# Performance work log

Hardware: AMD Instinct MI355X
Metric: run time of the kernel (lower is better)

The kernel has to match this reference:

```python
import jax, jax.numpy as jnp
import numpy as np

DIM, HEADS, K_MAX, K_MIN = 512, 8, 32, 4
DH = DIM // HEADS


def _conv1x1(x, w, b=None):
    # 1x1 Conv2d == pointwise linear over channels: [B,C,H,W] x [O,C] -> [B,O,H,W]
    y = jnp.einsum('bchw,oc->bohw', x, w)
    if b is not None:
        y = y + b[None, :, None, None]
    return y


def setup_inputs() -> dict:
    key = jax.random.key(0)
    ks = jax.random.split(key, 8)
    B, C, H, W = 2, DIM, 64, 64
    s = lambda fan: 1.0 / np.sqrt(fan)
    x = jax.random.normal(ks[0], (B, C, H, W), jnp.float32)
    w_qkv = jax.random.normal(ks[1], (3 * C, C), jnp.float32) * s(C)   # qkv conv, bias=False
    w_proj = jax.random.normal(ks[2], (C, C), jnp.float32) * s(C)      # proj conv
    b_proj = jax.random.normal(ks[3], (C,), jnp.float32) * s(C)
    w_g1 = jax.random.normal(ks[4], (C // 4, C), jnp.float32) * s(C)   # gate conv 1
    b_g1 = jax.random.normal(ks[5], (C // 4,), jnp.float32) * s(C)
    w_g2 = jax.random.normal(ks[6], (1, C // 4), jnp.float32) * s(C // 4)  # gate conv 2
    b_g2 = jnp.full((1,), -1.0, jnp.float32)  # nn.init.constant_(gate[-2].bias, -1.0)
    return {"x": x, "w_qkv": w_qkv, "w_proj": w_proj, "b_proj": b_proj,
            "w_g1": w_g1, "b_g1": b_g1, "w_g2": w_g2, "b_g2": b_g2}


def reference(x, w_qkv, w_proj, b_proj, w_g1, b_g1, w_g2, b_g2):
    B, C, H, W = x.shape
    N = H * W
    qkv = _conv1x1(x, w_qkv)                              # [B,3C,H,W]
    q, k, v = jnp.split(qkv, 3, axis=1)

    def rs(t):  # [B,C,H,W] -> [B,heads,N,dh]
        return t.reshape(B, HEADS, DH, N).transpose(0, 1, 3, 2)

    q, k, v = rs(q), rs(k), rs(v)
    sim = jnp.einsum('bhid,bhjd->bhij', q, k) / np.sqrt(DH)  # [B,h,N,N]

    # adaptive tau gate -> per-query dynamic k
    tau = jax.nn.sigmoid(_conv1x1(jax.nn.relu(_conv1x1(x, w_g1, b_g1)), w_g2, b_g2))
    tau = tau.reshape(B, 1, N)
    k_dyn = jnp.clip((tau * K_MAX).astype(jnp.int32), K_MIN, K_MAX)  # [B,1,N]

    topk_val, topk_idx = jax.lax.top_k(sim, K_MAX)         # [B,h,N,K], sorted descending
    mask = jnp.arange(K_MAX)[None, None, None, :] < k_dyn[..., None]  # [B,1,N,K] (bcast over h)
    topk_val = jnp.where(mask, topk_val, -jnp.inf)
    attn = jax.nn.softmax(topk_val, axis=-1)               # [B,h,N,K]

    # gather values: gathered[b,h,i,kk,:] = v[b,h,topk_idx[b,h,i,kk],:]
    bi = jnp.arange(B)[:, None, None, None]
    hi = jnp.arange(HEADS)[None, :, None, None]
    gathered = v[bi, hi, topk_idx]                         # [B,h,N,K,dh]
    out = jnp.einsum('bhnk,bhnkd->bhnd', attn, gathered)   # [B,h,N,dh]

    out = out.transpose(0, 1, 3, 2).reshape(B, C, H, W)
    out = _conv1x1(out, w_proj, b_proj)                    # proj (proj_drop=0)
    return x + out
```

## Files before the change

### kernel.cpp

```cpp
#include <hip/hip_runtime.h>
#include <math.h>

#define XSTRIDE  2097152u
#define G1STRIDE 524288u

typedef _Float16 f16;
typedef f16   f16x8  __attribute__((ext_vector_type(8)));
typedef float f32x16 __attribute__((ext_vector_type(16)));
typedef unsigned int u32;
typedef unsigned short u16;

#define WS_QH 0u
#define WS_QL 2097152u
#define WS_KH 4194304u
#define WS_KL 6291456u
#define WS_VB 8388608u
#define WS_G1 10485760u
#define WS_KD 11534336u
#define WS_CI 11542528u

template<int EPI>
__global__ __launch_bounds__(256)
void gemm_kernel(const float* __restrict__ A, const float* __restrict__ B,
                 const float* __restrict__ bias, const float* __restrict__ resid,
                 void* P0, void* P1, void* P2, void* P3, void* P4)
{
    const int tid = threadIdx.x;
    const int tm = tid & 15;
    const int tn = tid >> 4;
    const int m0 = blockIdx.y * 128;
    const int n0 = blockIdx.x * 128;
    const int b  = blockIdx.z;

    const float* Bb = B + (size_t)b * XSTRIDE;

    __shared__ float As[16][132];
    __shared__ float Bs[16][132];

    float acc[8][8];
    #pragma unroll
    for (int i = 0; i < 8; ++i)
        #pragma unroll
        for (int j = 0; j < 8; ++j) acc[i][j] = 0.0f;

    for (int k0 = 0; k0 < 512; k0 += 16) {
        {
            int id = tid * 2;
            #pragma unroll
            for (int r = 0; r < 2; ++r, ++id) {
                int m = id >> 2, kq = (id & 3) * 4;
                float4 v = *(const float4*)(A + (size_t)(m0 + m) * 512 + k0 + kq);
                As[kq + 0][m] = v.x; As[kq + 1][m] = v.y;
                As[kq + 2][m] = v.z; As[kq + 3][m] = v.w;
            }
        }
        if (EPI != 2) {
            int id = tid * 2;
            #pragma unroll
            for (int r = 0; r < 2; ++r, ++id) {
                int kk = id >> 5, nq = (id & 31) * 4;
                *(float4*)(&Bs[kk][nq]) =
                    *(const float4*)(Bb + (size_t)(k0 + kk) * 4096 + n0 + nq);
            }
        } else {
            const float* O0p = (const float*)P1;
            const float* O1p = (const float*)P2;
            const int hh = k0 >> 6, d0 = k0 & 63;
            int id = tid * 2;
            #pragma unroll
            for (int r = 0; r < 2; ++r, ++id) {
                int n = id >> 2, kq = (id & 3) * 4;
                int dd = d0 + kq;
                size_t rowp = ((size_t)((b * 8 + hh) * 4096) + n0 + n) * 32;
                const float* src = (dd < 32) ? (O0p + rowp + dd) : (O1p + rowp + dd - 32);
                float4 v = *(const float4*)src;
                Bs[kq + 0][n] = v.x; Bs[kq + 1][n] = v.y;
                Bs[kq + 2][n] = v.z; Bs[kq + 3][n] = v.w;
            }
        }
        __syncthreads();
        #pragma unroll
        for (int k = 0; k < 16; ++k) {
            float4 a0 = *(const float4*)(&As[k][tm * 8]);
            float4 a1 = *(const float4*)(&As[k][tm * 8 + 4]);
            float4 b0 = *(const float4*)(&Bs[k][tn * 8]);
            float4 b1 = *(const float4*)(&Bs[k][tn * 8 + 4]);
            float a[8] = {a0.x, a0.y, a0.z, a0.w, a1.x, a1.y, a1.z, a1.w};
            float bb[8] = {b0.x, b0.y, b0.z, b0.w, b1.x, b1.y, b1.z, b1.w};
            #pragma unroll
            for (int i = 0; i < 8; ++i)
                #pragma unroll
                for (int j = 0; j < 8; ++j)
                    acc[i][j] += a[i] * bb[j];
        }
        __syncthreads();
    }

    if (EPI == 2) {
        float* out = (float*)P0;
        #pragma unroll
        for (int i = 0; i < 8; ++i) {
            int o = m0 + tm * 8 + i;
            float bi = bias[o];
            size_t off = (size_t)b * XSTRIDE + (size_t)o * 4096 + n0 + tn * 8;
            float4 r0 = *(const float4*)(resid + off);
            float4 r1 = *(const float4*)(resid + off + 4);
            *(float4*)(out + off) = make_float4(acc[i][0] + bi + r0.x, acc[i][1] + bi + r0.y,
                                                acc[i][2] + bi + r0.z, acc[i][3] + bi + r0.w);
            *(float4*)(out + off + 4) = make_float4(acc[i][4] + bi + r1.x, acc[i][5] + bi + r1.y,
                                                    acc[i][6] + bi + r1.z, acc[i][7] + bi + r1.w);
        }
    }
}

__global__ __launch_bounds__(256)
void gate1_kernel(const float* __restrict__ A,
                  const float* __restrict__ B,
                  const float* __restrict__ bias,
                  float* __restrict__ G1)
{
    const int tid = threadIdx.x;
    const int tm = tid & 15;
    const int tn = tid >> 4;
    const int n0 = blockIdx.x * 32;
    const int b  = blockIdx.z;
    const float* Bb = B + (size_t)b * XSTRIDE;

    __shared__ float As[16][132];
    __shared__ float Bs[16][34];

    float acc[8][2];
    #pragma unroll
    for (int i = 0; i < 8; ++i) { acc[i][0] = 0.0f; acc[i][1] = 0.0f; }

    for (int k0 = 0; k0 < 512; k0 += 16) {
        {
            int id = tid * 2;
            #pragma unroll
            for (int r = 0; r < 2; ++r, ++id) {
                int m = id >> 2, kq = (id & 3) * 4;
                float4 v = *(const float4*)(A + (size_t)m * 512 + k0 + kq);
                As[kq + 0][m] = v.x; As[kq + 1][m] = v.y;
                As[kq + 2][m] = v.z; As[kq + 3][m] = v.w;
            }
        }
        {
            int kk = tid >> 4;
            int nn = (tid & 15) * 2;
            float2 v = *(const float2*)(Bb + (size_t)(k0 + kk) * 4096 + n0 + nn);
            Bs[kk][nn] = v.x; Bs[kk][nn + 1] = v.y;
        }
        __syncthreads();
        #pragma unroll
        for (int k = 0; k < 16; ++k) {
            float4 a0 = *(const float4*)(&As[k][tm * 8]);
            float4 a1 = *(const float4*)(&As[k][tm * 8 + 4]);
            float a[8] = {a0.x, a0.y, a0.z, a0.w, a1.x, a1.y, a1.z, a1.w};
            float b0 = Bs[k][tn * 2], b1 = Bs[k][tn * 2 + 1];
            #pragma unroll
            for (int i = 0; i < 8; ++i) {
                acc[i][0] += a[i] * b0;
                acc[i][1] += a[i] * b1;
            }
        }
        __syncthreads();
    }

    #pragma unroll
    for (int i = 0; i < 8; ++i) {
        int o = tm * 8 + i;
        float bi = bias[o];
        float* dst = G1 + (size_t)b * G1STRIDE + (size_t)o * 4096 + n0 + tn * 2;
        dst[0] = fmaxf(acc[i][0] + bi, 0.0f);
        dst[1] = fmaxf(acc[i][1] + bi, 0.0f);
    }
}

__global__ __launch_bounds__(256)
void convert_kernel(const float* __restrict__ x,
                    f16* __restrict__ XTH, f16* __restrict__ XTL)
{
    __shared__ float T[64][65];
    const int b = blockIdx.z;
    const int n0 = blockIdx.x * 64, k0 = blockIdx.y * 64;
    const int tid = threadIdx.x;
    const float* xb = x + (size_t)b * XSTRIDE;

    {
        const int c = tid & 63, r = tid >> 6;
        #pragma unroll
        for (int i = 0; i < 16; ++i)
            T[r + i * 4][c] = xb[(size_t)(k0 + r + i * 4) * 4096 + n0 + c];
    }
    __syncthreads();
    const int n = tid >> 2, a = tid & 3;
    f16x8 vh[2], vl[2];
    #pragma unroll
    for (int p = 0; p < 2; ++p)
        #pragma unroll
        for (int j = 0; j < 8; ++j) {
            float v = T[a * 16 + p * 8 + j][n];
            f16 h = (f16)v;
            vh[p][j] = h;
            vl[p][j] = (f16)((v - (float)h) * 4096.0f);
        }
    size_t dst = ((size_t)(b * 4096) + n0 + n) * 512 + k0 + a * 16;
    *(f16x8*)(XTH + dst)     = vh[0];
    *(f16x8*)(XTH + dst + 8) = vh[1];
    *(f16x8*)(XTL + dst)     = vl[0];
    *(f16x8*)(XTL + dst + 8) = vl[1];
}

__global__ __launch_bounds__(256, 2)
void qkv_gemm(const float* __restrict__ W, const f16* __restrict__ XTH,
              const f16* __restrict__ XTL,
              f16* __restrict__ QH, f16* __restrict__ QL,
              f16* __restrict__ KH, f16* __restrict__ KL,
              f16* __restrict__ VB)
{
    __shared__ __align__(16) char smem[33792];
    f16* Ah = (f16*)smem;
    f16* Al = (f16*)(smem + 6144);
    f16* Bh = (f16*)(smem + 12288);
    f16* Bl = (f16*)(smem + 18432);

    const int tid  = threadIdx.x;
    const int wid  = tid >> 6, lane = tid & 63;
    const int ln   = lane & 31, g = lane >> 5;
    const int wm   = wid >> 1, wn = wid & 1;
    const int m0   = blockIdx.y * 128;
    const int n0   = blockIdx.x * 128;
    const int b    = blockIdx.z;

    const int sm = tid >> 1, sko = (tid & 1) * 8;
    const float* wsrc  = W + (size_t)(m0 + sm) * 512 + sko;
    const f16*  bsrcH = XTH + ((size_t)(b * 4096) + n0 + sm) * 512 + sko;
    const f16*  bsrcL = XTL + ((size_t)(b * 4096) + n0 + sm) * 512 + sko;

    f32x16 accH[2][2], accL[2][2];
    #pragma unroll
    for (int rb = 0; rb < 2; ++rb)
        #pragma unroll
        for (int cb = 0; cb < 2; ++cb)
            #pragma unroll
            for (int r = 0; r < 16; ++r) { accH[rb][cb][r] = 0.0f; accL[rb][cb][r] = 0.0f; }

    for (int k0 = 0; k0 < 512; k0 += 16) {
        {
            float4 v0 = *(const float4*)(wsrc + k0);
            float4 v1 = *(const float4*)(wsrc + k0 + 4);
            float vv[8] = {v0.x, v0.y, v0.z, v0.w, v1.x, v1.y, v1.z, v1.w};
            f16x8 hh, ll;
            #pragma unroll
            for (int j = 0; j < 8; ++j) {
                f16 h = (f16)vv[j];
                hh[j] = h;
                ll[j] = (f16)((vv[j] - (float)h) * 4096.0f);
            }
            *(f16x8*)(Ah + sm * 24 + sko) = hh;
            *(f16x8*)(Al + sm * 24 + sko) = ll;
            *(f16x8*)(Bh + sm * 24 + sko) = *(const f16x8*)(bsrcH + k0);
            *(f16x8*)(Bl + sm * 24 + sko) = *(const f16x8*)(bsrcL + k0);
        }
        __syncthreads();
        f16x8 a_h[2], a_l[2], b_h[2], b_l[2];
        #pragma unroll
        for (int rb = 0; rb < 2; ++rb) {
            int row = wm * 64 + rb * 32 + ln;
            a_h[rb] = *(const f16x8*)(Ah + row * 24 + g * 8);
            a_l[rb] = *(const f16x8*)(Al + row * 24 + g * 8);
        }
        #pragma unroll
        for (int cb = 0; cb < 2; ++cb) {
            int col = wn * 64 + cb * 32 + ln;
            b_h[cb] = *(const f16x8*)(Bh + col * 24 + g * 8);
            b_l[cb] = *(const f16x8*)(Bl + col * 24 + g * 8);
        }
        #pragma unroll
        for (int rb = 0; rb < 2; ++rb)
            #pragma unroll
            for (int cb = 0; cb < 2; ++cb) {
                accH[rb][cb] = __builtin_amdgcn_mfma_f32_32x32x16_f16(a_h[rb], b_h[cb], accH[rb][cb], 0, 0, 0);
                accL[rb][cb] = __builtin_amdgcn_mfma_f32_32x32x16_f16(a_h[rb], b_l[cb], accL[rb][cb], 0, 0, 0);
                accL[rb][cb] = __builtin_amdgcn_mfma_f32_32x32x16_f16(a_l[rb], b_h[cb], accL[rb][cb], 0, 0, 0);
            }
        __syncthreads();
    }

    const int which = m0 >> 9;
    const float scale = (which == 0) ? 0.125f : 1.0f;
    const int hh_ = ((m0 & 511) >> 6) + wm;
    const size_t rowb0 = (size_t)(b * 8 + hh_) * 4096 + n0 + wn * 64 + lane;
    float* E = (float*)smem + wid * 2112;

    #pragma unroll
    for (int rb = 0; rb < 2; ++rb) {
        #pragma unroll
        for (int cb = 0; cb < 2; ++cb)
            #pragma unroll
            for (int r = 0; r < 16; ++r) {
                int row = (r & 3) + 8 * (r >> 2) + 4 * g;
                E[row * 66 + cb * 32 + ln] =
                    accH[rb][cb][r] + accL[rb][cb][r] * (1.0f / 4096.0f);
            }
        __syncthreads();
        const int dbase = rb * 32;
        if (which == 2) {
            #pragma unroll
            for (int oct = 0; oct < 4; ++oct) {
                f16x8 vv;
                #pragma unroll
                for (int j = 0; j < 8; ++j) vv[j] = (f16)E[(oct * 8 + j) * 66 + lane];
                *(f16x8*)(VB + rowb0 * 64 + dbase + oct * 8) = vv;
            }
        } else {
            f16* DH = which ? KH : QH;
            f16* DL = which ? KL : QL;
            #pragma unroll
            for (int oct = 0; oct < 4; ++oct) {
                f16x8 vh, vl;
                #pragma unroll
                for (int j = 0; j < 8; ++j) {
                    float xx = E[(oct * 8 + j) * 66 + lane] * scale;
                    f16 h = (f16)xx;
                    vh[j] = h;
                    vl[j] = (f16)((xx - (float)h) * 4096.0f);
                }
                *(f16x8*)(DH + rowb0 * 64 + dbase + oct * 8) = vh;
                *(f16x8*)(DL + rowb0 * 64 + dbase + oct * 8) = vl;
            }
        }
        __syncthreads();
    }
}

__global__ __launch_bounds__(64)
void gate2_kernel(const float* __restrict__ G1, const float* __restrict__ w2,
                  const float* __restrict__ b2, int* __restrict__ KD)
{
    const int b = blockIdx.y;
    const int n = blockIdx.x * 64 + threadIdx.x;
    const float* g = G1 + (size_t)b * G1STRIDE + n;
    float z = b2[0];
    #pragma unroll 8
    for (int c = 0; c < 128; ++c) z += w2[c] * g[(size_t)c * 4096];
    float tau = 1.0f / (1.0f + expf(-z));
    int kd = (int)(tau * 32.0f);
    kd = min(32, max(4, kd));
    KD[b * 4096 + n] = kd;
}

#define LOAD_BF(B0,B1,B2,B3,B4,B5,B6,B7, KHP, KLP, CB) do {                   \
    const f16* _ph = (KHP) + (size_t)((CB) * 32 + ln) * 64 + g * 8;           \
    const f16* _pl = (KLP) + (size_t)((CB) * 32 + ln) * 64 + g * 8;           \
    B0 = *(const f16x8*)(_ph);      B1 = *(const f16x8*)(_ph + 16);           \
    B2 = *(const f16x8*)(_ph + 32); B3 = *(const f16x8*)(_ph + 48);           \
    B4 = *(const f16x8*)(_pl);      B5 = *(const f16x8*)(_pl + 16);           \
    B6 = *(const f16x8*)(_pl + 32); B7 = *(const f16x8*)(_pl + 48);           \
} while (0)

#define P1_SCAN() do {                                                        \
    u32 _m = 0;                                                               \
    _Pragma("unroll")                                                         \
    for (int _q = 0; _q < 16; ++_q) {                                         \
        float2 _v = *(const float2*)(srow + 2 * _q);                          \
        _m |= (_v.x > thr) ? (1u << (2 * _q)) : 0u;                           \
        _m |= (_v.y > thr) ? (1u << (2 * _q + 1)) : 0u;                       \
    }                                                                         \
    while (__ballot(_m != 0u)) {                                              \
        bool _act = (_m != 0u);                                               \
        int _j = __builtin_ctz(_m ? _m : 1u);                                 \
        float _c = _act ? srow[_j] : 0.0f;                                    \
        _m &= (_m - 1u);                                                      \
        if (_act && _c > thr) {                                               \
            _Pragma("unroll")                                                 \
            for (int _r = 31; _r >= 1; --_r)                                  \
                L[_r] = __builtin_amdgcn_fmed3f(_c, L[_r - 1], L[_r]);        \
            L[0] = fmaxf(L[0], _c);                                           \
        }                                                                     \
    }                                                                         \
    {                                                                         \
        float _th = L[31];                                                    \
        _Pragma("unroll")                                                     \
        for (int _r = 30; _r >= 0; --_r) _th = (kdm1 == _r) ? L[_r] : _th;    \
        thr = _th;                                                            \
    }                                                                         \
} while (0)

#define P2_SCAN(JBASE) do {                                                   \
    u32 _m = 0;                                                               \
    _Pragma("unroll")                                                         \
    for (int _q = 0; _q < 16; ++_q) {                                         \
        float2 _v = *(const float2*)(srow + 2 * _q);                          \
        _m |= (_v.x >= theta) ? (1u << (2 * _q)) : 0u;                        \
        _m |= (_v.y >= theta) ? (1u << (2 * _q + 1)) : 0u;                    \
    }                                                                         \
    while (__ballot(_m != 0u)) {                                              \
        bool _act = (_m != 0u);                                               \
        int _j = __builtin_ctz(_m ? _m : 1u);                                 \
        float _c = _act ? srow[_j] : 0.0f;                                    \
        _m &= (_m - 1u);                                                      \
        if (_act) {                                                           \
            bool _isGT = _c > theta;                                          \
            bool _doA = (_isGT || eqc < eqNeed) && cnt < 32;                  \
            if (_doA) {                                                       \
                cvp[cnt] = _c;                                                \
                cip[cnt] = (u16)((JBASE) + _j);                               \
                cnt++;                                                        \
                if (!_isGT) eqc++;                                            \
            }                                                                 \
        }                                                                     \
    }                                                                         \
} while (0)

__device__ __forceinline__ void score_from(
    f16x8 bh0, f16x8 bh1, f16x8 bh2, f16x8 bh3,
    f16x8 bl0, f16x8 bl1, f16x8 bl2, f16x8 bl3,
    const f16x8 ah[2][4], const f16x8 al[2][4],
    float* __restrict__ Ss, int ln, int g)
{
    __builtin_amdgcn_s_setprio(1);
    #pragma unroll
    for (int rb = 0; rb < 2; ++rb) {
        f32x16 acc, accL;
        #pragma unroll
        for (int r = 0; r < 16; ++r) { acc[r] = 0.0f; accL[r] = 0.0f; }
        acc  = __builtin_amdgcn_mfma_f32_32x32x16_f16(ah[rb][0], bh0, acc,  0, 0, 0);
        accL = __builtin_amdgcn_mfma_f32_32x32x16_f16(al[rb][0], bh0, accL, 0, 0, 0);
        accL = __builtin_amdgcn_mfma_f32_32x32x16_f16(ah[rb][0], bl0, accL, 0, 0, 0);
        acc  = __builtin_amdgcn_mfma_f32_32x32x16_f16(ah[rb][1], bh1, acc,  0, 0, 0);
        accL = __builtin_amdgcn_mfma_f32_32x32x16_f16(al[rb][1], bh1, accL, 0, 0, 0);
        accL = __builtin_amdgcn_mfma_f32_32x32x16_f16(ah[rb][1], bl1, accL, 0, 0, 0);
        acc  = __builtin_amdgcn_mfma_f32_32x32x16_f16(ah[rb][2], bh2, acc,  0, 0, 0);
        accL = __builtin_amdgcn_mfma_f32_32x32x16_f16(al[rb][2], bh2, accL, 0, 0, 0);
        accL = __builtin_amdgcn_mfma_f32_32x32x16_f16(ah[rb][2], bl2, accL, 0, 0, 0);
        acc  = __builtin_amdgcn_mfma_f32_32x32x16_f16(ah[rb][3], bh3, acc,  0, 0, 0);
        accL = __builtin_amdgcn_mfma_f32_32x32x16_f16(al[rb][3], bh3, accL, 0, 0, 0);
        accL = __builtin_amdgcn_mfma_f32_32x32x16_f16(ah[rb][3], bl3, accL, 0, 0, 0);
        #pragma unroll
        for (int r = 0; r < 16; ++r) {
            int riw = rb * 32 + (r & 3) + 8 * (r >> 2) + 4 * g;
            Ss[riw * 34 + ln] = acc[r] + accL[r] * (1.0f / 4096.0f);
        }
    }
    __builtin_amdgcn_s_setprio(0);
}

__global__ __launch_bounds__(64)
__attribute__((amdgpu_waves_per_eu(2, 2)))
void select_kernel(const f16* __restrict__ QH, const f16* __restrict__ QL,
                   const f16* __restrict__ KH, const f16* __restrict__ KL,
                   const int* __restrict__ KD,
                   float* __restrict__ CV, u16* __restrict__ CI)
{
    const int qt = blockIdx.x >> 1;
    const int hf = blockIdx.x & 1;
    const int h = blockIdx.y, b = blockIdx.z;
    const size_t base = (size_t)((b * 8 + h) * 4096) * 64;
    const int lane = threadIdx.x;
    const int ln = lane & 31, g = lane >> 5;
    const int nw = qt * 64;
    const int k0base = hf * 2048;

    const int kd = KD[b * 4096 + nw + lane];
    const int kdm1 = kd - 1;

    __shared__ float Ss[64 * 34];

    f16x8 ah[2][4], al[2][4];
    #pragma unroll
    for (int rb = 0; rb < 2; ++rb) {
        const f16* ph = QH + base + (size_t)(nw + rb * 32 + ln) * 64 + g * 8;
        const f16* pl = QL + base + (size_t)(nw + rb * 32 + ln) * 64 + g * 8;
        #pragma unroll
        for (int s = 0; s < 4; ++s) {
            ah[rb][s] = *(const f16x8*)(ph + s * 16);
            al[rb][s] = *(const f16x8*)(pl + s * 16);
        }
    }

    const float INF = __builtin_inff();
    const float* srow = &Ss[lane * 34];

    f16x8 c0, c1, c2, c3, c4, c5, c6, c7;
    f16x8 n0, n1, n2, n3, n4, n5, n6, n7;

    float L[32];
    #pragma unroll
    for (int r = 0; r < 32; ++r) L[r] = -INF;
    float thr = -INF;

    {
        const f16* kh0 = KH + base + (size_t)k0base * 64;
        const f16* kl0 = KL + base + (size_t)k0base * 64;
        LOAD_BF(c0, c1, c2, c3, c4, c5, c6, c7, kh0, kl0, 0);
        for (int t = 0; t < 32; ++t) {
            const f16* kh_t = KH + base + (size_t)(k0base + t * 64) * 64;
            const f16* kl_t = KL + base + (size_t)(k0base + t * 64) * 64;
            const int t1 = (t < 31) ? t + 1 : 31;
            const f16* kh_n = KH + base + (size_t)(k0base + t1 * 64) * 64;
            const f16* kl_n = KL + base + (size_t)(k0base + t1 * 64) * 64;
            LOAD_BF(n0, n1, n2, n3, n4, n5, n6, n7, kh_t, kl_t, 1);
            score_from(c0, c1, c2, c3, c4, c5, c6, c7, ah, al, Ss, ln, g);
            P1_SCAN();
            LOAD_BF(c0, c1, c2, c3, c4, c5, c6, c7, kh_n, kl_n, 0);
            score_from(n0, n1, n2, n3, n4, n5, n6, n7, ah, al, Ss, ln, g);
            P1_SCAN();
        }
    }
    const float theta = thr;
    int cntGT = 0;
    #pragma unroll
    for (int r = 0; r < 32; ++r) cntGT += ((r < kd) && (L[r] > theta)) ? 1 : 0;
    const int eqNeed = kd - cntGT;

    const size_t crow = (size_t)((b * 8 + h) * 4096 + nw + lane);
    float* cvp = CV + crow * 64 + hf * 32;
    u16*   cip = CI + crow * 64 + hf * 32;
    int cnt = 0, eqc = 0;

    {
        const f16* kh0 = KH + base + (size_t)k0base * 64;
        const f16* kl0 = KL + base + (size_t)k0base * 64;
        LOAD_BF(c0, c1, c2, c3, c4, c5, c6, c7, kh0, kl0, 0);
        for (int t = 0; t < 32; ++t) {
            const f16* kh_t = KH + base + (size_t)(k0base + t * 64) * 64;
            const f16* kl_t = KL + base + (size_t)(k0base + t * 64) * 64;
            const int t1 = (t < 31) ? t + 1 : 31;
            const f16* kh_n = KH + base + (size_t)(k0base + t1 * 64) * 64;
            const f16* kl_n = KL + base + (size_t)(k0base + t1 * 64) * 64;
            LOAD_BF(n0, n1, n2, n3, n4, n5, n6, n7, kh_t, kl_t, 1);
            score_from(c0, c1, c2, c3, c4, c5, c6, c7, ah, al, Ss, ln, g);
            P2_SCAN(k0base + t * 64);
            LOAD_BF(c0, c1, c2, c3, c4, c5, c6, c7, kh_n, kl_n, 0);
            score_from(n0, n1, n2, n3, n4, n5, n6, n7, ah, al, Ss, ln, g);
            P2_SCAN(k0base + t * 64 + 32);
        }
    }
}

__global__ __launch_bounds__(64)
void merge_kernel(const float* __restrict__ CV, const u16* __restrict__ CI,
                  const int* __restrict__ KD, const f16* __restrict__ VB,
                  float* __restrict__ O0, float* __restrict__ O1)
{
    const int tid = threadIdx.x;
    const size_t R0 = (size_t)blockIdx.x * 64;

    __shared__ float Lv[64][66];
    __shared__ u16   Li[64][66];
    __shared__ float Mv[64][34];
    __shared__ u16   Mi[64][34];

    for (int i = 0; i < 64; ++i) {
        Lv[i][tid] = CV[(R0 + i) * 64 + tid];
        Li[i][tid] = CI[(R0 + i) * 64 + tid];
    }
    __syncthreads();

    const int myR = (int)R0 + tid;
    const int b = myR >> 15, n = myR & 4095, h = (myR >> 12) & 7;
    const int kd = KD[b * 4096 + n];

    const float INF = __builtin_inff();
    float L[32]; int I[32];
    #pragma unroll
    for (int r = 0; r < 32; ++r) { L[r] = -INF; I[r] = 0; }

    for (int i = 0; i < 64; ++i) {
        float c = Lv[tid][i];
        int  ix = Li[tid][i];
        if (c > L[31]) {
            #pragma unroll
            for (int r = 31; r >= 1; --r) {
                bool gp = c > L[r - 1];
                bool gc = c > L[r];
                L[r] = gp ? L[r - 1] : (gc ? c : L[r]);
                I[r] = gp ? I[r - 1] : (gc ? ix : I[r]);
            }
            if (c > L[0]) { I[0] = ix; L[0] = c; }
        }
    }

    #pragma unroll
    for (int r = 0; r < 32; ++r) { Mv[tid][r] = L[r]; Mi[tid][r] = (u16)I[r]; }

    const float mx = Mv[tid][0];
    float sum = 0.0f;
    for (int k = 0; k < kd; ++k) {
        float e = expf(Mv[tid][k] - mx);
        Mv[tid][k] = e;
        sum += e;
    }
    const float inv = 1.0f / sum;

    float o[64];
    #pragma unroll
    for (int d = 0; d < 64; ++d) o[d] = 0.0f;
    const size_t vbase = (size_t)((b * 8 + h)) * 4096 * 64;
    for (int k = 0; k < kd; ++k) {
        float wgt = Mv[tid][k] * inv;
        const f16* vp = VB + vbase + (size_t)Mi[tid][k] * 64;
        #pragma unroll
        for (int part = 0; part < 8; ++part) {
            f16x8 vv = *(const f16x8*)(vp + part * 8);
            #pragma unroll
            for (int e2 = 0; e2 < 8; ++e2) o[part * 8 + e2] += wgt * (float)vv[e2];
        }
    }

    __syncthreads();
    #pragma unroll
    for (int q = 0; q < 32; ++q)
        *(float2*)(&Lv[tid][2 * q]) = make_float2(o[2 * q], o[2 * q + 1]);
    __syncthreads();
    for (int i = 0; i < 64; ++i) {
        float val = Lv[i][tid];
        size_t R = R0 + i;
        if (tid < 32) O0[R * 32 + tid] = val;
        else          O1[R * 32 + (tid - 32)] = val;
    }
}

extern "C" void kernel_launch(void* const* d_in, const int* in_sizes, int n_in,
                              void* d_out, int out_size, void* d_ws, size_t ws_size,
                              hipStream_t stream)
{
    const float* x      = (const float*)d_in[0];
    const float* w_qkv  = (const float*)d_in[1];
    const float* w_proj = (const float*)d_in[2];
    const float* b_proj = (const float*)d_in[3];
    const float* w_g1   = (const float*)d_in[4];
    const float* b_g1   = (const float*)d_in[5];
    const float* w_g2   = (const float*)d_in[6];
    const float* b_g2   = (const float*)d_in[7];
    float* out = (float*)d_out;
    float* ws  = (float*)d_ws;

    f16* QH = (f16*)(ws + WS_QH);
    f16* QL = (f16*)(ws + WS_QL);
    f16* KH = (f16*)(ws + WS_KH);
    f16* KL = (f16*)(ws + WS_KL);
    f16* VB = (f16*)(ws + WS_VB);
    float* G1 = ws + WS_G1;
    int*   KD = (int*)(ws + WS_KD);
    u16*   CI = (u16*)(ws + WS_CI);
    float* CV = out;
    float* O0 = (float*)QH;
    float* O1 = (float*)QL;

    f16* XTH = (f16*)out;
    f16* XTL = (f16*)out + 4194304;

    convert_kernel<<<dim3(64, 8, 2), 256, 0, stream>>>(x, XTH, XTL);
    qkv_gemm<<<dim3(32, 12, 2), 256, 0, stream>>>(
        w_qkv, XTH, XTL, QH, QL, KH, KL, VB);
    gate1_kernel<<<dim3(128, 1, 2), 256, 0, stream>>>(w_g1, x, b_g1, G1);

    hipMemsetAsync(CV, 0xFF, (size_t)out_size * sizeof(float), stream);

    gate2_kernel<<<dim3(64, 2), 64, 0, stream>>>(G1, w_g2, b_g2, KD);
    select_kernel<<<dim3(128, 8, 2), 64, 0, stream>>>(QH, QL, KH, KL, KD, CV, CI);
    merge_kernel<<<dim3(1024), 64, 0, stream>>>(CV, CI, KD, VB, O0, O1);
    gemm_kernel<2><<<dim3(32, 4, 2), 256, 0, stream>>>(
        w_proj, nullptr, b_proj, x, out, O0, O1, nullptr, nullptr);
}
```

Before: 637.3 us.

## Move projection GEMM to split-fp16 MFMA and emit fp16 hi/lo from merge

Replaces the scalar fp32 projection GEMM with an MFMA 32x32x16 fp16 kernel that uses a hi/lo split (three MFMAs per tile) to keep near-fp32 accuracy. The merge kernel now writes its per-query outputs directly as token-major fp16 hi/lo pairs instead of staging through shared memory into two fp32 half-buffers. This is meant to cut the FMA-bound cost of the projection and simplify the merge store path. In exchange it adds an on-the-fly weight split per tile and a small precision change from the split representation.

```diff
diff --git a/kernel.cpp b/kernel.cpp
--- a/kernel.cpp
+++ b/kernel.cpp
@@ -18,100 +18,6 @@
 #define WS_G1 10485760u
 #define WS_KD 11534336u
 #define WS_CI 11542528u
-
-template<int EPI>
-__global__ __launch_bounds__(256)
-void gemm_kernel(const float* __restrict__ A, const float* __restrict__ B,
-                 const float* __restrict__ bias, const float* __restrict__ resid,
-                 void* P0, void* P1, void* P2, void* P3, void* P4)
-{
-    const int tid = threadIdx.x;
-    const int tm = tid & 15;
-    const int tn = tid >> 4;
-    const int m0 = blockIdx.y * 128;
-    const int n0 = blockIdx.x * 128;
-    const int b  = blockIdx.z;
-
-    const float* Bb = B + (size_t)b * XSTRIDE;
-
-    __shared__ float As[16][132];
-    __shared__ float Bs[16][132];
-
-    float acc[8][8];
-    #pragma unroll
-    for (int i = 0; i < 8; ++i)
-        #pragma unroll
-        for (int j = 0; j < 8; ++j) acc[i][j] = 0.0f;
-
-    for (int k0 = 0; k0 < 512; k0 += 16) {
-        {
-            int id = tid * 2;
-            #pragma unroll
-            for (int r = 0; r < 2; ++r, ++id) {
-                int m = id >> 2, kq = (id & 3) * 4;
-                float4 v = *(const float4*)(A + (size_t)(m0 + m) * 512 + k0 + kq);
-                As[kq + 0][m] = v.x; As[kq + 1][m] = v.y;
-                As[kq + 2][m] = v.z; As[kq + 3][m] = v.w;
-            }
-        }
-        if (EPI != 2) {
-            int id = tid * 2;
-            #pragma unroll
-            for (int r = 0; r < 2; ++r, ++id) {
-                int kk = id >> 5, nq = (id & 31) * 4;
-                *(float4*)(&Bs[kk][nq]) =
-                    *(const float4*)(Bb + (size_t)(k0 + kk) * 4096 + n0 + nq);
-            }
-        } else {
-            const float* O0p = (const float*)P1;
-            const float* O1p = (const float*)P2;
-            const int hh = k0 >> 6, d0 = k0 & 63;
-            int id = tid * 2;
-            #pragma unroll
-            for (int r = 0; r < 2; ++r, ++id) {
-                int n = id >> 2, kq = (id & 3) * 4;
-                int dd = d0 + kq;
-                size_t rowp = ((size_t)((b * 8 + hh) * 4096) + n0 + n) * 32;
-                const float* src = (dd < 32) ? (O0p + rowp + dd) : (O1p + rowp + dd - 32);
-                float4 v = *(const float4*)src;
-                Bs[kq + 0][n] = v.x; Bs[kq + 1][n] = v.y;
-                Bs[kq + 2][n] = v.z; Bs[kq + 3][n] = v.w;
-            }
-        }
-        __syncthreads();
-        #pragma unroll
-        for (int k = 0; k < 16; ++k) {
-            float4 a0 = *(const float4*)(&As[k][tm * 8]);
-            float4 a1 = *(const float4*)(&As[k][tm * 8 + 4]);
-            float4 b0 = *(const float4*)(&Bs[k][tn * 8]);
-            float4 b1 = *(const float4*)(&Bs[k][tn * 8 + 4]);
-            float a[8] = {a0.x, a0.y, a0.z, a0.w, a1.x, a1.y, a1.z, a1.w};
-            float bb[8] = {b0.x, b0.y, b0.z, b0.w, b1.x, b1.y, b1.z, b1.w};
-            #pragma unroll
-            for (int i = 0; i < 8; ++i)
-                #pragma unroll
-                for (int j = 0; j < 8; ++j)
-                    acc[i][j] += a[i] * bb[j];
-        }
-        __syncthreads();
-    }
-
-    if (EPI == 2) {
-        float* out = (float*)P0;
-        #pragma unroll
-        for (int i = 0; i < 8; ++i) {
-            int o = m0 + tm * 8 + i;
-            float bi = bias[o];
-            size_t off = (size_t)b * XSTRIDE + (size_t)o * 4096 + n0 + tn * 8;
-            float4 r0 = *(const float4*)(resid + off);
-            float4 r1 = *(const float4*)(resid + off + 4);
-            *(float4*)(out + off) = make_float4(acc[i][0] + bi + r0.x, acc[i][1] + bi + r0.y,
-                                                acc[i][2] + bi + r0.z, acc[i][3] + bi + r0.w);
-            *(float4*)(out + off + 4) = make_float4(acc[i][4] + bi + r1.x, acc[i][5] + bi + r1.y,
-                                                    acc[i][6] + bi + r1.z, acc[i][7] + bi + r1.w);
-        }
-    }
-}
 
 __global__ __launch_bounds__(256)
 void gate1_kernel(const float* __restrict__ A,
@@ -329,6 +235,103 @@
                 *(f16x8*)(DH + rowb0 * 64 + dbase + oct * 8) = vh;
                 *(f16x8*)(DL + rowb0 * 64 + dbase + oct * 8) = vl;
             }
+        }
+        __syncthreads();
+    }
+}
+
+__global__ __launch_bounds__(256, 2)
+void proj_gemm(const float* __restrict__ W, const f16* __restrict__ OH,
+               const f16* __restrict__ OL, const float* __restrict__ bias,
+               const float* __restrict__ resid, float* __restrict__ out)
+{
+    __shared__ __align__(16) char smem[33792];
+    f16* Ah = (f16*)smem;
+    f16* Al = (f16*)(smem + 6144);
+    f16* Bh = (f16*)(smem + 12288);
+    f16* Bl = (f16*)(smem + 18432);
+
+    const int tid  = threadIdx.x;
+    const int wid  = tid >> 6, lane = tid & 63;
+    const int ln   = lane & 31, g = lane >> 5;
+    const int wm   = wid >> 1, wn = wid & 1;
+    const int m0   = blockIdx.y * 128;
+    const int n0   = blockIdx.x * 128;
+    const int b    = blockIdx.z;
+
+    const int sm = tid >> 1, sko = (tid & 1) * 8;
+    const float* wsrc  = W + (size_t)(m0 + sm) * 512 + sko;
+    const f16*  bsrcH = OH + ((size_t)(b * 4096) + n0 + sm) * 512 + sko;
+    const f16*  bsrcL = OL + ((size_t)(b * 4096) + n0 + sm) * 512 + sko;
+
+    f32x16 accH[2][2], accL[2][2];
+    #pragma unroll
+    for (int rb = 0; rb < 2; ++rb)
+        #pragma unroll
+        for (int cb = 0; cb < 2; ++cb)
+            #pragma unroll
+            for (int r = 0; r < 16; ++r) { accH[rb][cb][r] = 0.0f; accL[rb][cb][r] = 0.0f; }
+
+    for (int k0 = 0; k0 < 512; k0 += 16) {
+        {
+            float4 v0 = *(const float4*)(wsrc + k0);
+            float4 v1 = *(const float4*)(wsrc + k0 + 4);
+            float vv[8] = {v0.x, v0.y, v0.z, v0.w, v1.x, v1.y, v1.z, v1.w};
+            f16x8 hh, ll;
+            #pragma unroll
+            for (int j = 0; j < 8; ++j) {
+                f16 h = (f16)vv[j];
+                hh[j] = h;
+                ll[j] = (f16)((vv[j] - (float)h) * 4096.0f);
+            }
+            *(f16x8*)(Ah + sm * 24 + sko) = hh;
+            *(f16x8*)(Al + sm * 24 + sko) = ll;
+            *(f16x8*)(Bh + sm * 24 + sko) = *(const f16x8*)(bsrcH + k0);
+            *(f16x8*)(Bl + sm * 24 + sko) = *(const f16x8*)(bsrcL + k0);
+        }
+        __syncthreads();
+        f16x8 a_h[2], a_l[2], b_h[2], b_l[2];
+        #pragma unroll
+        for (int rb = 0; rb < 2; ++rb) {
+            int row = wm * 64 + rb * 32 + ln;
+            a_h[rb] = *(const f16x8*)(Ah + row * 24 + g * 8);
+            a_l[rb] = *(const f16x8*)(Al + row * 24 + g * 8);
+        }
+        #pragma unroll
+        for (int cb = 0; cb < 2; ++cb) {
+            int col = wn * 64 + cb * 32 + ln;
+            b_h[cb] = *(const f16x8*)(Bh + col * 24 + g * 8);
+            b_l[cb] = *(const f16x8*)(Bl + col * 24 + g * 8);
+        }
+        #pragma unroll
+        for (int rb = 0; rb < 2; ++rb)
+            #pragma unroll
+            for (int cb = 0; cb < 2; ++cb) {
+                accH[rb][cb] = __builtin_amdgcn_mfma_f32_32x32x16_f16(a_h[rb], b_h[cb], accH[rb][cb], 0, 0, 0);
+                accL[rb][cb] = __builtin_amdgcn_mfma_f32_32x32x16_f16(a_h[rb], b_l[cb], accL[rb][cb], 0, 0, 0);
+                accL[rb][cb] = __builtin_amdgcn_mfma_f32_32x32x16_f16(a_l[rb], b_h[cb], accL[rb][cb], 0, 0, 0);
+            }
+        __syncthreads();
+    }
+
+    float* E = (float*)smem + wid * 2112;
+    #pragma unroll
+    for (int rb = 0; rb < 2; ++rb) {
+        #pragma unroll
+        for (int cb = 0; cb < 2; ++cb)
+            #pragma unroll
+            for (int r = 0; r < 16; ++r) {
+                int row = (r & 3) + 8 * (r >> 2) + 4 * g;
+                E[row * 66 + cb * 32 + ln] =
+                    accH[rb][cb][r] + accL[rb][cb][r] * (1.0f / 4096.0f);
+            }
+        __syncthreads();
+        #pragma unroll 4
+        for (int r = 0; r < 32; ++r) {
+            int o = m0 + wm * 64 + rb * 32 + r;
+            size_t off = (size_t)b * XSTRIDE + (size_t)o * 4096
+                       + n0 + wn * 64 + lane;
+            out[off] = E[r * 66 + lane] + bias[o] + resid[off];
         }
         __syncthreads();
     }
@@ -542,7 +545,7 @@
 __global__ __launch_bounds__(64)
 void merge_kernel(const float* __restrict__ CV, const u16* __restrict__ CI,
                   const int* __restrict__ KD, const f16* __restrict__ VB,
-                  float* __restrict__ O0, float* __restrict__ O1)
+                  f16* __restrict__ OH, f16* __restrict__ OL)
 {
     const int tid = threadIdx.x;
     const size_t R0 = (size_t)blockIdx.x * 64;
@@ -609,16 +612,19 @@
         }
     }
 
-    __syncthreads();
-    #pragma unroll
-    for (int q = 0; q < 32; ++q)
-        *(float2*)(&Lv[tid][2 * q]) = make_float2(o[2 * q], o[2 * q + 1]);
-    __syncthreads();
-    for (int i = 0; i < 64; ++i) {
-        float val = Lv[i][tid];
-        size_t R = R0 + i;
-        if (tid < 32) O0[R * 32 + tid] = val;
-        else          O1[R * 32 + (tid - 32)] = val;
+    const size_t obase = ((size_t)(b * 4096) + n) * 512 + h * 64;
+    #pragma unroll
+    for (int part = 0; part < 8; ++part) {
+        f16x8 vh, vl;
+        #pragma unroll
+        for (int e2 = 0; e2 < 8; ++e2) {
+            float v = o[part * 8 + e2];
+            f16 hh = (f16)v;
+            vh[e2] = hh;
+            vl[e2] = (f16)((v - (float)hh) * 4096.0f);
+        }
+        *(f16x8*)(OH + obase + part * 8) = vh;
+        *(f16x8*)(OL + obase + part * 8) = vl;
     }
 }
 
@@ -646,8 +652,8 @@
     int*   KD = (int*)(ws + WS_KD);
     u16*   CI = (u16*)(ws + WS_CI);
     float* CV = out;
-    float* O0 = (float*)QH;
-    float* O1 = (float*)QL;
+    f16* OH = (f16*)QH;
+    f16* OL = (f16*)QL;
 
     f16* XTH = (f16*)out;
     f16* XTL = (f16*)out + 4194304;
@@ -661,7 +667,7 @@
 
     gate2_kernel<<<dim3(64, 2), 64, 0, stream>>>(G1, w_g2, b_g2, KD);
     select_kernel<<<dim3(128, 8, 2), 64, 0, stream>>>(QH, QL, KH, KL, KD, CV, CI);
-    merge_kernel<<<dim3(1024), 64, 0, stream>>>(CV, CI, KD, VB, O0, O1);
-    gemm_kernel<2><<<dim3(32, 4, 2), 256, 0, stream>>>(
-        w_proj, nullptr, b_proj, x, out, O0, O1, nullptr, nullptr);
-}
+    merge_kernel<<<dim3(1024), 64, 0, stream>>>(CV, CI, KD, VB, OH, OL);
+    proj_gemm<<<dim3(32, 4, 2), 256, 0, stream>>>(
+        w_proj, OH, OL, b_proj, x, out);
+}
```

After: 605.9 us. -4.9%, faster.
